# Optimization experiments

Measured on AMD Instinct MI355X. Metric: run time of the kernel, lower is better.

The kernel has to match this reference:

```python
import jax, jax.numpy as jnp
import numpy as np

B, S, D, H, E = 4, 2048, 1024, 4096, 8


def setup_inputs() -> dict:
    key = jax.random.key(0)
    ks = jax.random.split(key, 8)
    w = lambda k, shape: (jax.random.normal(k, shape, jnp.float32) * 0.02)
    return {
        "x": jax.random.normal(ks[0], (B, S, D), jnp.float32),
        "noise_eps": jax.random.normal(ks[1], (B, S, E), jnp.float32),
        "Wg": w(ks[2], (D, E)), "bg": jnp.zeros((E,), jnp.float32),
        "Wn": w(ks[3], (D, E)), "bn": jnp.zeros((E,), jnp.float32),
        "W1": w(ks[4], (E, D, H)), "b1": jnp.zeros((E, H), jnp.float32),
        "W2": w(ks[5], (E, H, D)), "b2": jnp.zeros((E, D), jnp.float32),
        "top_k": 2,
    }


def reference(x, noise_eps, Wg, bg, Wn, bn, W1, b1, W2, b2, top_k):
    b, s, d = x.shape
    e = Wg.shape[1]
    xt = x.reshape(-1, d)            # [T, D] flattened tokens
    eps = noise_eps.reshape(-1, e)   # [T, E]

    # Noisy top-k router
    logits = xt @ Wg + bg                                   # [T, E]
    noisy = logits + eps * jax.nn.softplus(xt @ Wn + bn)    # [T, E]
    top_vals, top_idx = jax.lax.top_k(noisy, top_k)         # [T, k]

    # sparse logits: -inf everywhere except top-k, then softmax -> 0 gate off-topk
    rows = jnp.arange(xt.shape[0])[:, None]
    sparse = jnp.full_like(noisy, -jnp.inf).at[rows, top_idx].set(top_vals)
    gate = jax.nn.softmax(sparse, axis=-1)                  # [T, E], zeros off-topk

    # Expert MLPs (exact GELU, as nn.GELU default); gate==0 off-topk reproduces
    # the masked gather/scatter combine of the original exactly.
    out = jnp.zeros_like(xt)
    for i in range(e):  # small fixed expert count
        h = jax.nn.gelu(xt @ W1[i] + b1[i], approximate=False)  # [T, H]
        o = h @ W2[i] + b2[i]                                   # [T, D]
        out = out + o * gate[:, i:i + 1]
    return out.reshape(b, s, d)
```

## Files before the change

### kernel.cpp

```cpp
#include <hip/hip_runtime.h>
#include <hip/hip_bf16.h>
#include <cmath>

#define T_TOK 8192
#define E_NUM 8
#define D_DIM 1024
#define H_DIM 4096

typedef __attribute__((ext_vector_type(4))) short bf16x4;
typedef __attribute__((ext_vector_type(8))) short bf16x8;
typedef __attribute__((ext_vector_type(4))) float f32x4;

__device__ __forceinline__ unsigned short f2bf(float f) {
  union { float f; unsigned u; } v; v.f = f;
  unsigned r = v.u + 0x7fffu + ((v.u >> 16) & 1u);
  return (unsigned short)(r >> 16);
}

__global__ void __launch_bounds__(256) cvt_x_kernel(const float* __restrict__ x,
                                                    ushort* __restrict__ xb) {
  int i = blockIdx.x * 256 + threadIdx.x;
  float4 v = ((const float4*)x)[i];
  ushort4 o;
  o.x = f2bf(v.x); o.y = f2bf(v.y); o.z = f2bf(v.z); o.w = f2bf(v.w);
  ((ushort4*)xb)[i] = o;
}

__global__ void __launch_bounds__(256) transpose_cvt_kernel(
    const float* __restrict__ src, ushort* __restrict__ dst, int K, int N) {
  __shared__ float tile[32][33];
  size_t eoff = (size_t)blockIdx.z * K * N;
  src += eoff; dst += eoff;
  int n0 = blockIdx.x * 32, k0 = blockIdx.y * 32;
  int tx = threadIdx.x & 31, ty = threadIdx.x >> 5;
  for (int i = 0; i < 32; i += 8)
    tile[ty + i][tx] = src[(size_t)(k0 + ty + i) * N + n0 + tx];
  __syncthreads();
  for (int i = 0; i < 32; i += 8)
    dst[(size_t)(n0 + ty + i) * K + k0 + tx] = f2bf(tile[tx][ty + i]);
}

__global__ void __launch_bounds__(256) router_kernel(
    const float* __restrict__ x, const float* __restrict__ eps,
    const float* __restrict__ Wg, const float* __restrict__ bg,
    const float* __restrict__ Wn, const float* __restrict__ bn,
    int* __restrict__ tok, float* __restrict__ gateL, int* __restrict__ cnt) {
  int lane = threadIdx.x & 63;
  int t = blockIdx.x * 4 + (threadIdx.x >> 6);
  float ag[8], an[8];
#pragma unroll
  for (int e = 0; e < 8; ++e) { ag[e] = 0.f; an[e] = 0.f; }
  const float* xr = x + (size_t)t * D_DIM;
#pragma unroll 4
  for (int i = 0; i < 16; ++i) {
    int d = lane + i * 64;
    float xv = xr[d];
    const float4* g4 = (const float4*)(Wg + d * 8);
    const float4* n4 = (const float4*)(Wn + d * 8);
    float4 ga = g4[0], gb = g4[1], na = n4[0], nb = n4[1];
    ag[0] += xv * ga.x; ag[1] += xv * ga.y; ag[2] += xv * ga.z; ag[3] += xv * ga.w;
    ag[4] += xv * gb.x; ag[5] += xv * gb.y; ag[6] += xv * gb.z; ag[7] += xv * gb.w;
    an[0] += xv * na.x; an[1] += xv * na.y; an[2] += xv * na.z; an[3] += xv * na.w;
    an[4] += xv * nb.x; an[5] += xv * nb.y; an[6] += xv * nb.z; an[7] += xv * nb.w;
  }
#pragma unroll
  for (int off = 32; off > 0; off >>= 1) {
#pragma unroll
    for (int e = 0; e < 8; ++e) {
      ag[e] += __shfl_xor(ag[e], off);
      an[e] += __shfl_xor(an[e], off);
    }
  }
  if (lane == 0) {
    float noisy[8];
#pragma unroll
    for (int e = 0; e < 8; ++e) {
      float lg = ag[e] + bg[e];
      float ln = an[e] + bn[e];
      float sp = (ln > 20.f) ? ln : log1pf(expf(ln));
      noisy[e] = lg + eps[(size_t)t * 8 + e] * sp;
    }
    int i0 = 0; float v0 = noisy[0];
#pragma unroll
    for (int e = 1; e < 8; ++e) if (noisy[e] > v0) { v0 = noisy[e]; i0 = e; }
    int i1 = -1; float v1 = -1e30f;
#pragma unroll
    for (int e = 0; e < 8; ++e) if (e != i0 && noisy[e] > v1) { v1 = noisy[e]; i1 = e; }
    float ee = expf(v1 - v0);
    float g0 = 1.f / (1.f + ee);
    float g1 = ee / (1.f + ee);
    int p0 = atomicAdd(cnt + i0, 1);
    int p1 = atomicAdd(cnt + i1, 1);
    tok[i0 * T_TOK + p0] = t * 2;     gateL[i0 * T_TOK + p0] = g0;
    tok[i1 * T_TOK + p1] = t * 2 + 1; gateL[i1 * T_TOK + p1] = g1;
  }
}

template <int KD, int NC, bool FIRST>
__global__ void __launch_bounds__(256) moe_gemm_kernel(
    const ushort* __restrict__ Abase, const ushort* __restrict__ Bt,
    const float* __restrict__ bias, const int* __restrict__ tok,
    const float* __restrict__ gateL, const int* __restrict__ cnt,
    ushort* __restrict__ hbuf, float* __restrict__ out) {
  int e = blockIdx.z;
  int c = cnt[e];
  int m0 = blockIdx.y * 128;
  if (m0 >= c) return;
  int n0 = blockIdx.x * 128;
  __shared__ __align__(16) ushort As[128][72];
  __shared__ __align__(16) ushort Bs[128][72];
  int tid = threadIdx.x;
  int lane = tid & 63, wave = tid >> 6;
  int wr = (wave >> 1) * 64, wc = (wave & 1) * 64;
  const int* tokE = tok + e * T_TOK;
  const ushort* Be = Bt + (size_t)e * NC * KD;

  const ushort* agp[4]; const ushort* bgp[4];
  ushort* alp[4]; ushort* blp[4];
#pragma unroll
  for (int s = 0; s < 4; ++s) {
    int idx = tid + s * 256;
    int row = idx >> 3;
    int cg = (idx & 7) * 8;
    int p = m0 + row;
    int ar = 0;
    if (p < c) { int tsv = tokE[p]; ar = FIRST ? (tsv >> 1) : tsv; }
    agp[s] = Abase + (size_t)ar * KD + cg;
    bgp[s] = Be + (size_t)(n0 + row) * KD + cg;
    alp[s] = &As[row][cg];
    blp[s] = &Bs[row][cg];
  }

  f32x4 acc[4][4];
#pragma unroll
  for (int i = 0; i < 4; ++i)
#pragma unroll
    for (int j = 0; j < 4; ++j) {
      f32x4 z = {0.f, 0.f, 0.f, 0.f};
      acc[i][j] = z;
    }

  int r16 = lane & 15;
  int kh = (lane >> 4) << 2;

  for (int kt = 0; kt < KD / 64; ++kt) {
    __syncthreads();
#pragma unroll
    for (int s = 0; s < 4; ++s) {
      *(bf16x8*)alp[s] = *(const bf16x8*)(agp[s] + kt * 64);
      *(bf16x8*)blp[s] = *(const bf16x8*)(bgp[s] + kt * 64);
    }
    __syncthreads();
#pragma unroll
    for (int ks = 0; ks < 2; ++ks) {
      bf16x8 af[4], bfr[4];
#pragma unroll
      for (int i = 0; i < 4; ++i) {
        union { bf16x8 v8; bf16x4 v4[2]; } ua, ub;
        const ushort* ap = &As[wr + i * 16 + r16][ks * 32 + kh];
        ua.v4[0] = *(const bf16x4*)ap;
        ua.v4[1] = *(const bf16x4*)(ap + 16);
        af[i] = ua.v8;
        const ushort* bp = &Bs[wc + i * 16 + r16][ks * 32 + kh];
        ub.v4[0] = *(const bf16x4*)bp;
        ub.v4[1] = *(const bf16x4*)(bp + 16);
        bfr[i] = ub.v8;
      }
#pragma unroll
      for (int mi = 0; mi < 4; ++mi)
#pragma unroll
        for (int ni = 0; ni < 4; ++ni)
          acc[mi][ni] = __builtin_amdgcn_mfma_f32_16x16x32_bf16(
              af[mi], bfr[ni], acc[mi][ni], 0, 0, 0);
    }
  }

  const float* be = bias + (size_t)e * NC;
#pragma unroll
  for (int mi = 0; mi < 4; ++mi) {
#pragma unroll
    for (int r = 0; r < 4; ++r) {
      int rowl = wr + mi * 16 + ((lane >> 4) << 2) + r;
      int p = m0 + rowl;
      if (p < c) {
        int tsv = tokE[p];
        if (FIRST) {
          ushort* hrow = hbuf + (size_t)tsv * H_DIM;
#pragma unroll
          for (int ni = 0; ni < 4; ++ni) {
            int col = n0 + wc + ni * 16 + r16;
            float v = acc[mi][ni][r] + be[col];
            v = 0.5f * v * (1.f + erff(v * 0.70710678118654752f));
            hrow[col] = f2bf(v);
          }
        } else {
          float g = gateL[e * T_TOK + p];
          float* orow = out + (size_t)(tsv >> 1) * D_DIM;
#pragma unroll
          for (int ni = 0; ni < 4; ++ni) {
            int col = n0 + wc + ni * 16 + r16;
            float v = acc[mi][ni][r] + be[col];
            atomicAdd(&orow[col], g * v);
          }
        }
      }
    }
  }
}

extern "C" void kernel_launch(void* const* d_in, const int* in_sizes, int n_in,
                              void* d_out, int out_size, void* d_ws, size_t ws_size,
                              hipStream_t stream) {
  const float* x   = (const float*)d_in[0];
  const float* eps = (const float*)d_in[1];
  const float* Wg  = (const float*)d_in[2];
  const float* bg  = (const float*)d_in[3];
  const float* Wn  = (const float*)d_in[4];
  const float* bn  = (const float*)d_in[5];
  const float* W1  = (const float*)d_in[6];
  const float* b1  = (const float*)d_in[7];
  const float* W2  = (const float*)d_in[8];
  const float* b2  = (const float*)d_in[9];
  float* out = (float*)d_out;

  const size_t nXB = (size_t)T_TOK * D_DIM;
  const size_t nW1 = (size_t)E_NUM * D_DIM * H_DIM;
  const size_t nHB = (size_t)T_TOK * 2 * H_DIM;
  ushort* xb   = (ushort*)d_ws;
  ushort* W1T  = xb + nXB;
  ushort* W2T  = W1T + nW1;
  ushort* hbuf = W2T + nW1;
  int*   tok   = (int*)(hbuf + nHB);
  float* gateL = (float*)(tok + E_NUM * T_TOK);
  int*   cnt   = (int*)(gateL + E_NUM * T_TOK);
  size_t need = (size_t)((char*)(cnt + 8) - (char*)d_ws);
  if (ws_size < need) return;

  hipMemsetAsync(cnt, 0, 8 * sizeof(int), stream);
  hipMemsetAsync(out, 0, (size_t)out_size * sizeof(float), stream);

  cvt_x_kernel<<<(int)(nXB / 4 / 256), 256, 0, stream>>>(x, xb);
  transpose_cvt_kernel<<<dim3(H_DIM / 32, D_DIM / 32, E_NUM), 256, 0, stream>>>(
      W1, W1T, D_DIM, H_DIM);
  transpose_cvt_kernel<<<dim3(D_DIM / 32, H_DIM / 32, E_NUM), 256, 0, stream>>>(
      W2, W2T, H_DIM, D_DIM);
  router_kernel<<<T_TOK / 4, 256, 0, stream>>>(x, eps, Wg, bg, Wn, bn, tok, gateL, cnt);
  moe_gemm_kernel<D_DIM, H_DIM, true>
      <<<dim3(H_DIM / 128, T_TOK / 128, E_NUM), 256, 0, stream>>>(
          xb, W1T, b1, tok, gateL, cnt, hbuf, out);
  moe_gemm_kernel<H_DIM, D_DIM, false>
      <<<dim3(D_DIM / 128, T_TOK / 128, E_NUM), 256, 0, stream>>>(
          hbuf, W2T, b2, tok, gateL, cnt, hbuf, out);
}
```

Before: 1.350 ms.

## Use direct global-to-LDS loads with XOR swizzle and XCD-aware block remap

Replaces register-staged global-to-LDS copies with global_load_lds 16-byte direct loads into an unpadded LDS tile. Bank conflicts are avoided with an XOR swizzle on 16-byte chunks. The 3D grid becomes a 1D grid, and block ids are remapped so consecutive workgroups on the same XCD share expert and column tiles for better L2 reuse. This cuts VGPR traffic and load latency, but it depends on the 16-byte global_load_lds variant and on a correct lane-to-LDS ordering.

```diff
diff --git a/kernel.cpp b/kernel.cpp
--- a/kernel.cpp
+++ b/kernel.cpp
@@ -15,6 +15,12 @@
   union { float f; unsigned u; } v; v.f = f;
   unsigned r = v.u + 0x7fffu + ((v.u >> 16) & 1u);
   return (unsigned short)(r >> 16);
+}
+
+__device__ __forceinline__ void gload_lds16(const void* g, void* l) {
+  __builtin_amdgcn_global_load_lds(
+      (const __attribute__((address_space(1))) unsigned int*)g,
+      (__attribute__((address_space(3))) unsigned int*)l, 16, 0, 0);
 }
 
 __global__ void __launch_bounds__(256) cvt_x_kernel(const float* __restrict__ x,
@@ -102,33 +108,40 @@
     const float* __restrict__ bias, const int* __restrict__ tok,
     const float* __restrict__ gateL, const int* __restrict__ cnt,
     ushort* __restrict__ hbuf, float* __restrict__ out) {
-  int e = blockIdx.z;
+  constexpr int MT = T_TOK / 128;
+  constexpr int NT = NC / 128;
+  int nwg = MT * NT * E_NUM;
+  int q = nwg >> 3;
+  int bid = blockIdx.x;
+  int wg = (bid & 7) * q + (bid >> 3);
+  int m_t = wg % MT;
+  int n_t = (wg / MT) % NT;
+  int e = wg / (MT * NT);
+
   int c = cnt[e];
-  int m0 = blockIdx.y * 128;
+  int m0 = m_t * 128;
   if (m0 >= c) return;
-  int n0 = blockIdx.x * 128;
-  __shared__ __align__(16) ushort As[128][72];
-  __shared__ __align__(16) ushort Bs[128][72];
+  int n0 = n_t * 128;
+
+  __shared__ __align__(16) ushort As[128 * 64];
+  __shared__ __align__(16) ushort Bs[128 * 64];
   int tid = threadIdx.x;
   int lane = tid & 63, wave = tid >> 6;
   int wr = (wave >> 1) * 64, wc = (wave & 1) * 64;
   const int* tokE = tok + e * T_TOK;
   const ushort* Be = Bt + (size_t)e * NC * KD;
 
-  const ushort* agp[4]; const ushort* bgp[4];
-  ushort* alp[4]; ushort* blp[4];
-#pragma unroll
-  for (int s = 0; s < 4; ++s) {
-    int idx = tid + s * 256;
-    int row = idx >> 3;
-    int cg = (idx & 7) * 8;
-    int p = m0 + row;
+  int srow = tid >> 3, scol = tid & 7;
+  const ushort* asrc[4]; const ushort* bsrc[4];
+#pragma unroll
+  for (int p = 0; p < 4; ++p) {
+    int r = p * 32 + srow;
+    int pi = m0 + r;
     int ar = 0;
-    if (p < c) { int tsv = tokE[p]; ar = FIRST ? (tsv >> 1) : tsv; }
-    agp[s] = Abase + (size_t)ar * KD + cg;
-    bgp[s] = Be + (size_t)(n0 + row) * KD + cg;
-    alp[s] = &As[row][cg];
-    blp[s] = &Bs[row][cg];
+    if (pi < c) { int tsv = tokE[pi]; ar = FIRST ? (tsv >> 1) : tsv; }
+    int sl = (scol ^ (r & 7)) * 8;
+    asrc[p] = Abase + (size_t)ar * KD + sl;
+    bsrc[p] = Be + (size_t)(n0 + r) * KD + sl;
   }
 
   f32x4 acc[4][4];
@@ -141,29 +154,33 @@
     }
 
   int r16 = lane & 15;
-  int kh = (lane >> 4) << 2;
+  int kh8 = (lane >> 4) * 8;
+  int swz = (r16 & 7) << 4;
 
   for (int kt = 0; kt < KD / 64; ++kt) {
     __syncthreads();
 #pragma unroll
-    for (int s = 0; s < 4; ++s) {
-      *(bf16x8*)alp[s] = *(const bf16x8*)(agp[s] + kt * 64);
-      *(bf16x8*)blp[s] = *(const bf16x8*)(bgp[s] + kt * 64);
-    }
+    for (int p = 0; p < 4; ++p)
+      gload_lds16(asrc[p] + kt * 64, (char*)As + p * 4096 + tid * 16);
+#pragma unroll
+    for (int p = 0; p < 4; ++p)
+      gload_lds16(bsrc[p] + kt * 64, (char*)Bs + p * 4096 + tid * 16);
     __syncthreads();
+
 #pragma unroll
     for (int ks = 0; ks < 2; ++ks) {
       bf16x8 af[4], bfr[4];
+      int k0 = ks * 64 + kh8;
 #pragma unroll
       for (int i = 0; i < 4; ++i) {
+        int rowA = (wr + i * 16 + r16) * 128;
         union { bf16x8 v8; bf16x4 v4[2]; } ua, ub;
-        const ushort* ap = &As[wr + i * 16 + r16][ks * 32 + kh];
-        ua.v4[0] = *(const bf16x4*)ap;
-        ua.v4[1] = *(const bf16x4*)(ap + 16);
+        ua.v4[0] = *(const bf16x4*)((const char*)As + rowA + (k0 ^ swz));
+        ua.v4[1] = *(const bf16x4*)((const char*)As + rowA + ((k0 + 32) ^ swz));
         af[i] = ua.v8;
-        const ushort* bp = &Bs[wc + i * 16 + r16][ks * 32 + kh];
-        ub.v4[0] = *(const bf16x4*)bp;
-        ub.v4[1] = *(const bf16x4*)(bp + 16);
+        int rowB = (wc + i * 16 + r16) * 128;
+        ub.v4[0] = *(const bf16x4*)((const char*)Bs + rowB + (k0 ^ swz));
+        ub.v4[1] = *(const bf16x4*)((const char*)Bs + rowB + ((k0 + 32) ^ swz));
         bfr[i] = ub.v8;
       }
 #pragma unroll
@@ -246,9 +263,9 @@
       W2, W2T, H_DIM, D_DIM);
   router_kernel<<<T_TOK / 4, 256, 0, stream>>>(x, eps, Wg, bg, Wn, bn, tok, gateL, cnt);
   moe_gemm_kernel<D_DIM, H_DIM, true>
-      <<<dim3(H_DIM / 128, T_TOK / 128, E_NUM), 256, 0, stream>>>(
+      <<<(T_TOK / 128) * (H_DIM / 128) * E_NUM, 256, 0, stream>>>(
           xb, W1T, b1, tok, gateL, cnt, hbuf, out);
   moe_gemm_kernel<H_DIM, D_DIM, false>
-      <<<dim3(D_DIM / 128, T_TOK / 128, E_NUM), 256, 0, stream>>>(
+      <<<(T_TOK / 128) * (D_DIM / 128) * E_NUM, 256, 0, stream>>>(
           hbuf, W2T, b2, tok, gateL, cnt, hbuf, out);
 }
```

New measurement: 1.131 ms. 16.2% less time.
